# Performance work log

Measured on AMD Instinct MI355X. Metric: run time of the kernel, lower is better.

The kernel has to match this reference:

```python
import jax, jax.numpy as jnp
import numpy as np

ALPHA, BETA, GAMMA = 0.05, 0.95, 0.95   # list_weight
TANH_ALPHA = 2.0
GDEP = 2


def _gcn_rnn(x, adp, preA, W, b):
    # GCN type 'RNN': adaptive batched adj + predefined adj
    h = x
    outs = [h]
    for _ in range(GDEP):
        h = (ALPHA * x
             + BETA * jnp.einsum('nvc,nvw->nwc', h, adp)
             + GAMMA * jnp.einsum('nvc,vw->nwc', h, preA))
        outs.append(h)
    return jnp.concatenate(outs, -1) @ W + b


def _gcn_hyper(x, A, W, b):
    h = x
    outs = [h]
    for _ in range(GDEP):
        h = ALPHA * x + GAMMA * jnp.einsum('nvc,vw->nwc', h, A)
        outs.append(h)
    return jnp.concatenate(outs, -1) @ W + b


def _gcn_tgn(x, Ab, W, b):
    h = x
    outs = [h]
    for _ in range(GDEP):
        h = ALPHA * x + GAMMA * jnp.einsum('nvc,nvw->nwc', h, Ab)
        outs.append(h)
    return jnp.concatenate(outs, -1) @ W + b


def setup_inputs() -> dict:
    key = jax.random.key(0)
    ks = jax.random.split(key, 28)
    B, T, N, F = 16, 24, 512, 2
    H, E = 64, 16          # hidden_size, node embedding dim (dims_hyper[-1])
    TGN_OUT = 32
    D_ATTN = 4 * F         # TAttn default dim_out = 4 * dim_in
    p = lambda i, shape: jax.random.normal(ks[i], shape, dtype=jnp.float32) * 0.1
    return {
        'sample': jax.random.normal(ks[0], (B, T, N, F), dtype=jnp.float32),
        'predefined_A': jax.random.uniform(ks[1], (N, N), dtype=jnp.float32),
        'w_query': p(2, (F, D_ATTN)), 'w_key': p(3, (F, D_ATTN)),
        'attn_bias': p(4, (D_ATTN,)), 'attn_trans': p(5, (D_ATTN, 1)),
        'W_tgn': p(6, ((GDEP + 1) * F, TGN_OUT)), 'b_tgn': p(7, (TGN_OUT,)),
        'W_agg1': p(8, ((GDEP + 1) * H, E)), 'b_agg1': p(9, (E,)),
        'W_agg2': p(10, ((GDEP + 1) * H, E)), 'b_agg2': p(11, (E,)),
        'W_srcemb': p(12, (F, E)), 'b_srcemb': p(13, (E,)),
        'W_tgtemb': p(14, (F, E)), 'b_tgtemb': p(15, (E,)),
        'W_gz': p(16, ((GDEP + 1) * (F + H), H)), 'b_gz': p(17, (H,)),
        'W_gr': p(18, ((GDEP + 1) * (F + H), H)), 'b_gr': p(19, (H,)),
        'W_gc': p(20, ((GDEP + 1) * (F + H), H)), 'b_gc': p(21, (H,)),
        'W_short': p(22, (TGN_OUT, F)), 'b_short': p(23, (F,)),
        'W_long': p(24, (H, F)), 'b_long': p(25, (F,)),
        'W_mix': p(26, (TGN_OUT + H, F)), 'b_mix': p(27, (F,)),
    }


def reference(sample, predefined_A, w_query, w_key, attn_bias, attn_trans,
              W_tgn, b_tgn, W_agg1, b_agg1, W_agg2, b_agg2,
              W_srcemb, b_srcemb, W_tgtemb, b_tgtemb,
              W_gz, b_gz, W_gr, b_gr, W_gc, b_gc,
              W_short, b_short, W_long, b_long, W_mix, b_mix):
    B, T, N, F = sample.shape
    H = W_long.shape[0]
    A = predefined_A
    eye = jnp.eye(N, dtype=sample.dtype)

    def gru_step(hidden, graph):
        # hidden: [B,N,H], graph: [B,N,F]
        gs = _gcn_hyper(hidden, A, W_agg1, b_agg1)
        gt = _gcn_hyper(hidden, A, W_agg2, b_agg2)
        nv_s = jnp.tanh(TANH_ALPHA * (graph @ W_srcemb + b_srcemb) * gs)
        nv_t = jnp.tanh(TANH_ALPHA * (graph @ W_tgtemb + b_tgtemb) * gt)
        a = (jnp.einsum('bnd,bmd->bnm', nv_s, nv_t)
             - jnp.einsum('bnd,bmd->bnm', nv_t, nv_s))
        adp = jax.nn.relu(jnp.tanh(TANH_ALPHA * a)) + eye
        adp = adp / adp.sum(-1, keepdims=True)           # row-normalized [B,N,N]
        combined = jnp.concatenate([graph, hidden], -1)
        z = jax.nn.sigmoid(_gcn_rnn(combined, adp, A, W_gz, b_gz))
        r = jax.nn.sigmoid(_gcn_rnn(combined, adp, A, W_gr, b_gr))
        c = jnp.tanh(_gcn_rnn(jnp.concatenate([graph, r * hidden], -1), adp, A, W_gc, b_gc))
        return z * hidden + (1.0 - z) * c

    hidden = jnp.zeros((B, N, H), dtype=sample.dtype)
    graphs = jnp.moveaxis(sample[:, 0:T - 4:4], 1, 0)    # [T', B, N, F]
    hidden = jax.lax.scan(lambda h, g: (gru_step(h, g), None), hidden, graphs)[0]

    # temporal additive attention over the last 4 graphs (TAttn)
    src = sample[:, -4:]                                  # [B,4,N,F]
    tar = sample[:, -1]                                   # [B,N,F]
    q = (tar @ w_query)[:, None, :, None, :]              # [B,1,N,1,D]
    k = (src @ w_key)[:, :, None, :, :]                   # [B,4,1,N,D]
    scores = (jnp.tanh(q + k + attn_bias) @ attn_trans)[..., 0]   # [B,4,N,N]
    attn = jax.nn.softmax(scores, axis=-1)

    # single TGN layer: graph conv with (predefined + attention) adjacency
    Ab = A[None] + attn.reshape(-1, N, N)                 # [B*4,N,N]
    out = _gcn_tgn(src.reshape(-1, N, F), Ab, W_tgn, b_tgn)
    out = jax.nn.relu(out.reshape(B, 4, N, -1))
    tar = out.sum(axis=1)                                 # [B,N,TGN_OUT]

    gat_result = tar @ W_short + b_short                  # [B,N,F]
    hidden = gru_step(hidden, gat_result)
    gru_result = hidden @ W_long + b_long
    final_result = jnp.concatenate([tar, hidden], -1) @ W_mix + b_mix
    return gat_result, gru_result, final_result, attn
```

## Files before the change

kernel.cpp:

```cpp
#include <hip/hip_runtime.h>

#define ALPHA_C 0.05f
#define BETA_C  0.95f
#define GAMMA_C 0.95f

constexpr int B = 16, T = 24, N = 512, F = 2, H = 64, E = 16;
constexpr int DA = 8;
constexpr int CC = F + H;
constexpr int TGN_OC = 32;
constexpr int NPART = 4;

__device__ __forceinline__ float fast_rcp(float x) { return __builtin_amdgcn_rcpf(x); }
__device__ __forceinline__ float fast_tanh(float x) {
    return 1.0f - 2.0f * fast_rcp(__expf(2.0f * x) + 1.0f);
}
__device__ __forceinline__ float fast_sigmoid(float x) {
    return fast_rcp(1.0f + __expf(-x));
}

__global__ void scaleA_kernel(const float* __restrict__ A, float* __restrict__ K1)
{
    int i = blockIdx.x * 256 + threadIdx.x;
    K1[i] = GAMMA_C * A[i];
}

__global__ __launch_bounds__(256) void k2_kernel(const float* __restrict__ A,
                                                 float* __restrict__ K2)
{
    __shared__ float rows[16][258];
    __shared__ float cols[256][17];
    const int tid = threadIdx.x;
    const int r0 = blockIdx.y * 16, c0 = blockIdx.x * 16;
    const int rr = tid >> 4, cc = tid & 15;
    float acc = 0.f;
    for (int k0 = 0; k0 < N; k0 += 256) {
#pragma unroll
        for (int it = 0; it < 4; ++it) {
            int l = it * 256 + tid;
            int row = l >> 6, k4 = (l & 63) << 2;
            *(float4*)&rows[row][k4] = *(const float4*)(A + (size_t)(r0 + row) * N + k0 + k4);
        }
#pragma unroll
        for (int it = 0; it < 4; ++it) {
            int l = it * 256 + tid;
            int k = l >> 2, c4 = (l & 3) << 2;
            *(float4*)&cols[k][c4] = *(const float4*)(A + (size_t)(k0 + k) * N + c0 + c4);
        }
        __syncthreads();
#pragma unroll 8
        for (int k = 0; k < 256; ++k) acc += rows[rr][k] * cols[k][cc];
        __syncthreads();
    }
    size_t i = (size_t)(r0 + rr) * N + c0 + cc;
    K2[i] = GAMMA_C * ALPHA_C * A[i] + GAMMA_C * GAMMA_C * acc;
}

template<int GCOLS, bool INSUM, bool MPB>
__device__ __forceinline__ void bmm_core(
    float* __restrict__ out, const float* __restrict__ x, const float* __restrict__ in,
    const float* __restrict__ M, int b, int w0, int vq, int tid,
    float (*sh_m)[68], float (*sh_h)[68])
{
    constexpr int Crow = 64 + GCOLS;
    const size_t pstr = (size_t)B * N * Crow;
    const int cg = tid & 15;
    const int wg = tid >> 4;

    float acc[2][4] = {{0,0,0,0},{0,0,0,0}};
    float ag[2] = {0.f, 0.f};

    const float* Mb = M + (MPB ? (size_t)b * N * N : 0);
    const float* inb = in + (size_t)b * N * Crow;

    for (int vt = 0; vt < 2; ++vt) {
        const int v0 = vq * 128 + vt * 64;
#pragma unroll
        for (int it = 0; it < 2; ++it) {
            int l = it * 512 + tid;
            int row = l >> 4, c4 = (l & 15) << 2;
            *(float4*)&sh_m[row][c4] =
                *(const float4*)(Mb + (size_t)(v0 + row) * N + w0 + c4);
        }
        if (GCOLS == 2) {
            const float2* h0 = (const float2*)(inb + (size_t)v0 * Crow);
            for (int l = tid; l < 64 * 33; l += 512) {
                int row = l / 33, k = (l - row * 33) * 2;
                float2 v = h0[l];
                if (INSUM) {
#pragma unroll
                    for (int j = 1; j < NPART; ++j) {
                        float2 w = ((const float2*)(inb + (size_t)j * pstr + (size_t)v0 * Crow))[l];
                        v.x += w.x; v.y += w.y;
                    }
                }
                *(float2*)&sh_h[row][k] = v;
            }
        } else {
            const float4* h0 = (const float4*)(inb + (size_t)v0 * Crow);
#pragma unroll
            for (int it = 0; it < 2; ++it) {
                int l = it * 512 + tid;
                int row = l >> 4, k = (l & 15) << 2;
                float4 v = h0[l];
                if (INSUM) {
#pragma unroll
                    for (int j = 1; j < NPART; ++j) {
                        float4 w = ((const float4*)(inb + (size_t)j * pstr + (size_t)v0 * Crow))[l];
                        v.x += w.x; v.y += w.y; v.z += w.z; v.w += w.w;
                    }
                }
                *(float4*)&sh_h[row][k] = v;
            }
        }
        __syncthreads();
#pragma unroll 8
        for (int j = 0; j < 64; ++j) {
            float2 mv = *(const float2*)&sh_m[j][wg << 1];
            float4 hv = *(const float4*)&sh_h[j][cg << 2];
            acc[0][0] += mv.x * hv.x; acc[0][1] += mv.x * hv.y;
            acc[0][2] += mv.x * hv.z; acc[0][3] += mv.x * hv.w;
            acc[1][0] += mv.y * hv.x; acc[1][1] += mv.y * hv.y;
            acc[1][2] += mv.y * hv.z; acc[1][3] += mv.y * hv.w;
            if (GCOLS > 0 && cg < GCOLS) {
                float gv = sh_h[j][64 + cg];
                ag[0] += mv.x * gv; ag[1] += mv.y * gv;
            }
        }
        __syncthreads();
    }
    float* outp = out + (size_t)vq * pstr + (size_t)b * N * Crow;
    const float* xb = x + (size_t)b * N * Crow;
#pragma unroll
    for (int r = 0; r < 2; ++r) {
        const int w = w0 + (wg << 1) + r;
        const size_t base = (size_t)w * Crow + (cg << 2);
        if (GCOLS == 2) {
            float o0 = acc[r][0], o1 = acc[r][1], o2 = acc[r][2], o3 = acc[r][3];
            if (vq == 0) {
                o0 += ALPHA_C * xb[base];     o1 += ALPHA_C * xb[base + 1];
                o2 += ALPHA_C * xb[base + 2]; o3 += ALPHA_C * xb[base + 3];
            }
            float2 lo = {o0, o1}, hi = {o2, o3};
            *(float2*)(outp + base) = lo;
            *(float2*)(outp + base + 2) = hi;
            if (cg < GCOLS) {
                size_t gb = (size_t)w * Crow + 64 + cg;
                float v = ag[r];
                if (vq == 0) v += ALPHA_C * xb[gb];
                outp[gb] = v;
            }
        } else {
            float4 ov = {acc[r][0], acc[r][1], acc[r][2], acc[r][3]};
            if (vq == 0) {
                float4 xv = *(const float4*)(xb + base);
                ov.x += ALPHA_C * xv.x; ov.y += ALPHA_C * xv.y;
                ov.z += ALPHA_C * xv.z; ov.w += ALPHA_C * xv.w;
            }
            *(float4*)(outp + base) = ov;
        }
    }
}

template<bool INSUM>
__global__ __launch_bounds__(512) void bmm4_kernel(
    float* __restrict__ out, const float* __restrict__ x, const float* __restrict__ in,
    const float* __restrict__ M)
{
    __shared__ float sh_m[64][68];
    __shared__ float sh_h[64][68];
    bmm_core<2, INSUM, true>(out, x, in, M, blockIdx.z, blockIdx.x * 64, blockIdx.y,
                             threadIdx.x, sh_m, sh_h);
}

__global__ __launch_bounds__(512) void hyper_kernel(
    float* __restrict__ P1, float* __restrict__ P2, const float* __restrict__ hidden,
    const float* __restrict__ K1, const float* __restrict__ K2)
{
    __shared__ float sh_m[64][68];
    __shared__ float sh_h[64][68];
    int vq = blockIdx.y & 3, which = blockIdx.y >> 2;
    float* out = which ? P2 : P1;
    const float* M = which ? K2 : K1;
    bmm_core<0, false, false>(out, hidden, hidden, M, blockIdx.z, blockIdx.x * 64, vq,
                              threadIdx.x, sh_m, sh_h);
}

__global__ __launch_bounds__(256) void gsgt5_kernel(
    const float* __restrict__ hidden, const float* __restrict__ P1, const float* __restrict__ P2,
    const float* __restrict__ Wa1, const float* __restrict__ ba1,
    const float* __restrict__ Wa2, const float* __restrict__ ba2,
    const float* __restrict__ graph, long gstride,
    const float* __restrict__ Wsrc, const float* __restrict__ bsrc,
    const float* __restrict__ Wtgt, const float* __restrict__ btgt,
    float* __restrict__ nv_s, float* __restrict__ nv_t)
{
    constexpr size_t psH = (size_t)B * N * H;
    __shared__ float sh[16][196];
    __shared__ float W1t[16][196];
    __shared__ float W2t[16][196];
    const int tid = threadIdx.x;
    const int e = tid & 15;
    const int row = tid >> 4;
    const size_t nn0 = (size_t)blockIdx.x * 16;
    {
        int f4 = ((int)(nn0) + row) * 16 + e;
        float4 v = ((const float4*)hidden)[f4];
        *(float4*)&sh[row][e << 2] = v;
        float4 a = ((const float4*)P1)[f4];
#pragma unroll
        for (int j = 1; j < NPART; ++j) {
            float4 w = ((const float4*)(P1 + (size_t)j * psH))[f4];
            a.x += w.x; a.y += w.y; a.z += w.z; a.w += w.w;
        }
        *(float4*)&sh[row][64 + (e << 2)] = a;
        float4 c = ((const float4*)P2)[f4];
#pragma unroll
        for (int j = 1; j < NPART; ++j) {
            float4 w = ((const float4*)(P2 + (size_t)j * psH))[f4];
            c.x += w.x; c.y += w.y; c.z += w.z; c.w += w.w;
        }
        *(float4*)&sh[row][128 + (e << 2)] = c;
    }
    for (int l = tid; l < 768; l += 256) {
        int sk = l >> 2, q = l & 3;
        float4 w1 = ((const float4*)Wa1)[l];
        float4 w2 = ((const float4*)Wa2)[l];
        W1t[4 * q + 0][sk] = w1.x; W1t[4 * q + 1][sk] = w1.y;
        W1t[4 * q + 2][sk] = w1.z; W1t[4 * q + 3][sk] = w1.w;
        W2t[4 * q + 0][sk] = w2.x; W2t[4 * q + 1][sk] = w2.y;
        W2t[4 * q + 2][sk] = w2.z; W2t[4 * q + 3][sk] = w2.w;
    }
    __syncthreads();
    float gs = ba1[e], gt = ba2[e];
#pragma unroll 8
    for (int sk = 0; sk < 192; sk += 4) {
        float4 xv = *(const float4*)&sh[row][sk];
        float4 w1 = *(const float4*)&W1t[e][sk];
        float4 w2 = *(const float4*)&W2t[e][sk];
        gs += xv.x * w1.x + xv.y * w1.y + xv.z * w1.z + xv.w * w1.w;
        gt += xv.x * w2.x + xv.y * w2.y + xv.z * w2.z + xv.w * w2.w;
    }
    size_t nn = nn0 + row;
    int b = (int)(nn >> 9), n = (int)(nn & (N - 1));
    const float* g = graph + (size_t)b * gstride + (size_t)n * F;
    float g0 = g[0], g1 = g[1];
    float es = g0 * Wsrc[e] + g1 * Wsrc[E + e] + bsrc[e];
    float et = g0 * Wtgt[e] + g1 * Wtgt[E + e] + btgt[e];
    nv_s[nn * E + e] = fast_tanh(2.0f * es * gs);
    nv_t[nn * E + e] = fast_tanh(2.0f * et * gt);
}

__global__ __launch_bounds__(512) void adp3_kernel(
    const float* __restrict__ nv_s, const float* __restrict__ nv_t,
    const float* __restrict__ A,
    const float* __restrict__ hidden, const float* __restrict__ graph, long gstride,
    float* __restrict__ Mcomb, float* __restrict__ comb)
{
    __shared__ float red[8][4];
    __shared__ float tot[4];
    const int m = threadIdx.x;
    const int n0 = blockIdx.x * 4;
    const int b = blockIdx.y;
    const float4* sm = (const float4*)(nv_s + ((size_t)b * N + m) * E);
    const float4* tm = (const float4*)(nv_t + ((size_t)b * N + m) * E);
    const float4* sn = (const float4*)(nv_s + ((size_t)b * N + n0) * E);
    const float4* tn = (const float4*)(nv_t + ((size_t)b * N + n0) * E);
    float a1[4] = {0.f,0.f,0.f,0.f}, a2[4] = {0.f,0.f,0.f,0.f};
#pragma unroll
    for (int dd = 0; dd < 4; ++dd) {
        float4 smv = sm[dd], tmv = tm[dd];
#pragma unroll
        for (int r = 0; r < 4; ++r) {
            float4 snv = sn[r * 4 + dd], tnv = tn[r * 4 + dd];
            a1[r] += snv.x * tmv.x + snv.y * tmv.y + snv.z * tmv.z + snv.w * tmv.w;
            a2[r] += tnv.x * smv.x + tnv.y * smv.y + tnv.z * smv.z + tnv.w * smv.w;
        }
    }
    float p[4];
#pragma unroll
    for (int r = 0; r < 4; ++r) {
        float pv = fmaxf(fast_tanh(2.0f * (a1[r] - a2[r])), 0.0f);
        if (m == n0 + r) pv += 1.0f;
        p[r] = pv;
    }
    float sr[4] = {p[0], p[1], p[2], p[3]};
    for (int o = 32; o > 0; o >>= 1) {
#pragma unroll
        for (int r = 0; r < 4; ++r) sr[r] += __shfl_down(sr[r], o);
    }
    int wid = m >> 6, lane = m & 63;
    if (lane == 0) {
#pragma unroll
        for (int r = 0; r < 4; ++r) red[wid][r] = sr[r];
    }
    __syncthreads();
    if (m < 4) {
        float t = 0.f;
        for (int i = 0; i < 8; ++i) t += red[i][m];
        tot[m] = BETA_C * fast_rcp(t);
    }
    __syncthreads();
#pragma unroll
    for (int r = 0; r < 4; ++r)
        Mcomb[((size_t)b * N + n0 + r) * N + m] =
            GAMMA_C * A[(size_t)(n0 + r) * N + m] + p[r] * tot[r];
    if (m < 4 * CC) {
        int r = m / CC, k = m - r * CC;
        size_t nn = (size_t)b * N + n0 + r;
        float v;
        if (k < F) v = graph[(size_t)b * gstride + (size_t)(n0 + r) * F + k];
        else       v = hidden[nn * H + (k - F)];
        comb[nn * CC + k] = v;
    }
}

__device__ __forceinline__ void stage_xt(float (*Xt)[20], const float* __restrict__ base,
                                         const float* __restrict__ P1,
                                         const float* __restrict__ P2,
                                         size_t nn0, int tid)
{
    constexpr size_t psC = (size_t)B * N * CC;
    const float2* c2 = (const float2*)(base + nn0 * CC);
    const float2* p1b = (const float2*)(P1 + nn0 * CC);
    const float2* p2b = (const float2*)(P2 + nn0 * CC);
    for (int l = tid; l < 16 * 33; l += 256) {
        int row = l & 15, kp = l >> 4;
        int idx = row * 33 + kp;
        float2 v = c2[idx];
        Xt[2 * kp][row] = v.x; Xt[2 * kp + 1][row] = v.y;
        float2 a = p1b[idx];
#pragma unroll
        for (int j = 1; j < NPART; ++j) {
            float2 w = ((const float2*)(P1 + (size_t)j * psC + nn0 * CC))[idx];
            a.x += w.x; a.y += w.y;
        }
        Xt[66 + 2 * kp][row] = a.x; Xt[66 + 2 * kp + 1][row] = a.y;
        float2 c = p2b[idx];
#pragma unroll
        for (int j = 1; j < NPART; ++j) {
            float2 w = ((const float2*)(P2 + (size_t)j * psC + nn0 * CC))[idx];
            c.x += w.x; c.y += w.y;
        }
        Xt[132 + 2 * kp][row] = c.x; Xt[132 + 2 * kp + 1][row] = c.y;
    }
}

__global__ __launch_bounds__(256) void zr5_kernel(
    const float* __restrict__ comb, const float* __restrict__ P1, const float* __restrict__ P2,
    const float* __restrict__ Wgz, const float* __restrict__ bgz,
    const float* __restrict__ Wgr, const float* __restrict__ bgr,
    const float* __restrict__ hidden,
    float* __restrict__ z, float* __restrict__ comb2)
{
    __shared__ float Xt[198][20];
    __shared__ float Wl[66][128];
    const int tid = threadIdx.x;
    const size_t nn0 = (size_t)blockIdx.x * 16;

    stage_xt(Xt, comb, P1, P2, nn0, tid);

    const int cp = tid & 63;
    const int rg = tid >> 6;
    float2 bias = (cp < 32) ? *(const float2*)&bgz[2 * cp]
                            : *(const float2*)&bgr[2 * cp - 64];
    float acc[4][2];
#pragma unroll
    for (int r = 0; r < 4; ++r) { acc[r][0] = bias.x; acc[r][1] = bias.y; }

    for (int ch = 0; ch < 3; ++ch) {
        const int sk0 = ch * 66;
        for (int l = tid; l < 66 * 32; l += 256) {
            int j = l >> 5, q = l & 31;
            float4 w = (q < 16)
                ? ((const float4*)(Wgz + (size_t)(sk0 + j) * H))[q]
                : ((const float4*)(Wgr + (size_t)(sk0 + j) * H))[q - 16];
            *(float4*)&Wl[j][q << 2] = w;
        }
        __syncthreads();
#pragma unroll 6
        for (int j = 0; j < 66; ++j) {
            float4 xv = *(const float4*)&Xt[sk0 + j][rg << 2];
            float2 wv = *(const float2*)&Wl[j][cp << 1];
            acc[0][0] += xv.x * wv.x; acc[0][1] += xv.x * wv.y;
            acc[1][0] += xv.y * wv.x; acc[1][1] += xv.y * wv.y;
            acc[2][0] += xv.z * wv.x; acc[2][1] += xv.z * wv.y;
            acc[3][0] += xv.w * wv.x; acc[3][1] += xv.w * wv.y;
        }
        __syncthreads();
    }

    if (cp < 32) {
        const int oc = 2 * cp;
#pragma unroll
        for (int r = 0; r < 4; ++r) {
            size_t nn = nn0 + (rg << 2) + r;
            z[nn * H + oc]     = fast_sigmoid(acc[r][0]);
            z[nn * H + oc + 1] = fast_sigmoid(acc[r][1]);
        }
    } else {
        const int oc = 2 * cp - 64;
#pragma unroll
        for (int r = 0; r < 4; ++r) {
            size_t nn = nn0 + (rg << 2) + r;
            float h0 = hidden[nn * H + oc], h1 = hidden[nn * H + oc + 1];
            comb2[nn * CC + F + oc]     = fast_sigmoid(acc[r][0]) * h0;
            comb2[nn * CC + F + oc + 1] = fast_sigmoid(acc[r][1]) * h1;
        }
    }
    if (tid < 32) {
        int row = tid >> 1, f = tid & 1;
        comb2[(nn0 + row) * CC + f] = Xt[f][row];
    }
}

__global__ __launch_bounds__(256) void cup5_kernel(
    const float* __restrict__ comb2, const float* __restrict__ P1, const float* __restrict__ P2,
    const float* __restrict__ Wgc, const float* __restrict__ bgc,
    const float* __restrict__ z, float* __restrict__ hidden)
{
    __shared__ float Xt[198][20];
    __shared__ float Wl[66][64];
    const int tid = threadIdx.x;
    const size_t nn0 = (size_t)blockIdx.x * 16;

    stage_xt(Xt, comb2, P1, P2, nn0, tid);

    const int cp = tid & 31;
    const int rg = tid >> 5;
    float2 bias = *(const float2*)&bgc[2 * cp];
    float acc[2][2];
#pragma unroll
    for (int r = 0; r < 2; ++r) { acc[r][0] = bias.x; acc[r][1] = bias.y; }

    for (int ch = 0; ch < 3; ++ch) {
        const int sk0 = ch * 66;
        for (int l = tid; l < 66 * 16; l += 256) {
            int j = l >> 4, q = l & 15;
            float4 w = ((const float4*)(Wgc + (size_t)(sk0 + j) * H))[q];
            *(float4*)&Wl[j][q << 2] = w;
        }
        __syncthreads();
#pragma unroll 6
        for (int j = 0; j < 66; ++j) {
            float2 xv = *(const float2*)&Xt[sk0 + j][rg << 1];
            float2 wv = *(const float2*)&Wl[j][cp << 1];
            acc[0][0] += xv.x * wv.x; acc[0][1] += xv.x * wv.y;
            acc[1][0] += xv.y * wv.x; acc[1][1] += xv.y * wv.y;
        }
        __syncthreads();
    }

    const int oc = 2 * cp;
#pragma unroll
    for (int r = 0; r < 2; ++r) {
        size_t nn = nn0 + (rg << 1) + r;
        float cv0 = fast_tanh(acc[r][0]);
        float cv1 = fast_tanh(acc[r][1]);
        float zv0 = z[nn * H + oc],     ho0 = hidden[nn * H + oc];
        float zv1 = z[nn * H + oc + 1], ho1 = hidden[nn * H + oc + 1];
        hidden[nn * H + oc]     = zv0 * ho0 + (1.0f - zv0) * cv0;
        hidden[nn * H + oc + 1] = zv1 * ho1 + (1.0f - zv1) * cv1;
    }
}

__global__ void qk_kernel(const float* __restrict__ sample,
                          const float* __restrict__ wq, const float* __restrict__ wk,
                          const float* __restrict__ attn_bias,
                          float* __restrict__ q, float* __restrict__ kk)
{
    int idx = blockIdx.x * 256 + threadIdx.x;
    if (idx < B * N * DA) {
        int d = idx & 7;
        int n = (idx >> 3) & (N - 1);
        int b = idx >> 12;
        const float* tar = sample + (((size_t)b * T + (T - 1)) * N + n) * F;
        q[idx] = tar[0] * wq[d] + tar[1] * wq[DA + d] + attn_bias[d];
    } else {
        int j = idx - B * N * DA;
        int d = j & 7;
        int n = (j >> 3) & (N - 1);
        int t = (j >> 12) & 3;
        int b = j >> 14;
        const float* s = sample + (((size_t)b * T + (T - 4 + t)) * N + n) * F;
        kk[j] = s[0] * wk[d] + s[1] * wk[DA + d];
    }
}

__global__ __launch_bounds__(256) void scores3_kernel(
    const float* __restrict__ q, const float* __restrict__ kk,
    const float* __restrict__ trans, float* __restrict__ attn)
{
    int bt = blockIdx.y;
    int b = bt >> 2;
    int rbase = blockIdx.x * 16;
    int wid = threadIdx.x >> 6, lane = threadIdx.x & 63;
    const float* kkbt = kk + (size_t)bt * N * DA;
    float* attnbt = attn + (size_t)bt * N * N;
    float tr[8];
#pragma unroll
    for (int d = 0; d < 8; ++d) tr[d] = trans[d];
    for (int i = 0; i < 4; ++i) {
        int n = rbase + wid * 4 + i;
        const float* qp = q + ((size_t)b * N + n) * DA;
        float4 qa = *(const float4*)qp, qb = *(const float4*)(qp + 4);
        float ev[8]; float ssum = 0.f;
#pragma unroll
        for (int k = 0; k < 8; ++k) {
            const float* kp = kkbt + (size_t)(k * 64 + lane) * DA;
            float4 ka = *(const float4*)kp, kb = *(const float4*)(kp + 4);
            float s = fast_tanh(qa.x + ka.x) * tr[0] + fast_tanh(qa.y + ka.y) * tr[1]
                    + fast_tanh(qa.z + ka.z) * tr[2] + fast_tanh(qa.w + ka.w) * tr[3]
                    + fast_tanh(qb.x + kb.x) * tr[4] + fast_tanh(qb.y + kb.y) * tr[5]
                    + fast_tanh(qb.z + kb.z) * tr[6] + fast_tanh(qb.w + kb.w) * tr[7];
            ev[k] = __expf(s);
            ssum += ev[k];
        }
        for (int o = 32; o > 0; o >>= 1) ssum += __shfl_down(ssum, o);
        ssum = __shfl(ssum, 0);
        float rinv = fast_rcp(ssum);
#pragma unroll
        for (int k = 0; k < 8; ++k)
            attnbt[(size_t)n * N + k * 64 + lane] = ev[k] * rinv;
    }
}

__global__ __launch_bounds__(256) void tgn2_kernel(
    const float* __restrict__ A, const float* __restrict__ attn,
    const float* __restrict__ hbase, long hsB, long hsT,
    const float* __restrict__ xbase, long xsB, long xsT,
    float* __restrict__ out)
{
    __shared__ float sh_m[64][65];
    __shared__ float sh_h[64][2];
    int bt = blockIdx.y;
    int w0 = blockIdx.x * 64;
    int tid = threadIdx.x;
    int wl = tid >> 2, c = tid & 1, vh = (tid >> 1) & 1;
    const float* hp = hbase + (size_t)(bt >> 2) * hsB + (size_t)(bt & 3) * hsT;
    const float* ap = attn + (size_t)bt * N * N;
    float acc = 0.f;
    for (int vt = 0; vt < 8; ++vt) {
        int v0 = vt * 64;
#pragma unroll
        for (int it = 0; it < 16; ++it) {
            int l = it * 256 + tid;
            int vr = l >> 6, wc = l & 63;
            size_t gi = (size_t)(v0 + vr) * N + (w0 + wc);
            sh_m[wc][vr] = A[gi] + ap[gi];
        }
        if (tid < 128) sh_h[tid >> 1][tid & 1] = hp[(size_t)(v0 + (tid >> 1)) * F + (tid & 1)];
        __syncthreads();
#pragma unroll
        for (int jj = 0; jj < 32; ++jj) {
            int j = vh * 32 + jj;
            acc += sh_m[wl][j] * sh_h[j][c];
        }
        __syncthreads();
    }
    acc += __shfl_xor(acc, 2);
    if (vh == 0) {
        const float* xp = xbase + (size_t)(bt >> 2) * xsB + (size_t)(bt & 3) * xsT;
        out[((size_t)bt * N + w0 + wl) * F + c] =
            ALPHA_C * xp[(size_t)(w0 + wl) * F + c] + GAMMA_C * acc;
    }
}

__global__ __launch_bounds__(256) void tgn_out_gat_kernel(
    const float* __restrict__ sample,
    const float* __restrict__ th1, const float* __restrict__ th2,
    const float* __restrict__ Wt, const float* __restrict__ bt_,
    const float* __restrict__ Ws, const float* __restrict__ bs,
    float* __restrict__ tar32, float* __restrict__ out0)
{
    __shared__ float sh_t[8][33];
    const int tid = threadIdx.x;
    const int oc = tid & 31;
    const int r = tid >> 5;
    const size_t nn = (size_t)blockIdx.x * 8 + r;
    const int n = (int)(nn & (N - 1));
    const int b = (int)(nn >> 9);
    float acc = 0.f;
    for (int t = 0; t < 4; ++t) {
        int bt = b * 4 + t;
        const float* s = sample + (((size_t)b * T + (T - 4 + t)) * N + n) * F;
        size_t rr = ((size_t)bt * N + n) * F;
        float v = bt_[oc];
        v += s[0] * Wt[0 * TGN_OC + oc] + s[1] * Wt[1 * TGN_OC + oc];
        v += th1[rr] * Wt[2 * TGN_OC + oc] + th1[rr + 1] * Wt[3 * TGN_OC + oc];
        v += th2[rr] * Wt[4 * TGN_OC + oc] + th2[rr + 1] * Wt[5 * TGN_OC + oc];
        acc += fmaxf(v, 0.0f);
    }
    tar32[nn * TGN_OC + oc] = acc;
    sh_t[r][oc] = acc;
    __syncthreads();
    if (tid < 16) {
        int row = tid >> 1, f = tid & 1;
        size_t nn2 = (size_t)blockIdx.x * 8 + row;
        float g = bs[f];
#pragma unroll
        for (int k = 0; k < TGN_OC; ++k) g += sh_t[row][k] * Ws[(size_t)k * F + f];
        out0[nn2 * F + f] = g;
    }
}

__global__ void final_kernel(const float* __restrict__ hidden, const float* __restrict__ tar32,
                             const float* __restrict__ Wl, const float* __restrict__ bl,
                             const float* __restrict__ Wm, const float* __restrict__ bm,
                             float* __restrict__ dout_gru, float* __restrict__ dout_fin)
{
    int idx = blockIdx.x * 256 + threadIdx.x;
    int f = idx & 1;
    int nn = idx >> 1;
    const float* hp = hidden + (size_t)nn * H;
    const float* tp = tar32 + (size_t)nn * TGN_OC;
    float g = bl[f], fin = bm[f];
    for (int k = 0; k < H; ++k) g += hp[k] * Wl[(size_t)k * F + f];
    for (int k = 0; k < TGN_OC; ++k) fin += tp[k] * Wm[(size_t)k * F + f];
    for (int k = 0; k < H; ++k) fin += hp[k] * Wm[(size_t)(TGN_OC + k) * F + f];
    dout_gru[idx] = g;
    dout_fin[idx] = fin;
}

namespace {
struct Ptrs {
    const float *sample, *A, *wq, *wk, *attn_bias, *attn_trans, *Wt, *bt_;
    const float *Wa1, *ba1, *Wa2, *ba2, *Wsrc, *bsrc, *Wtgt, *btgt;
    const float *Wgz, *bgz, *Wgr, *bgr, *Wgc, *bgc, *Wsh, *bsh, *Wl, *bl, *Wm, *bm;
    float *hidden, *nvs, *nvt, *Mcomb, *K1, *K2, *comb, *comb2, *z, *P1, *P2;
    float *q, *kk, *th1, *th2, *tar32;
};

void gru_step(hipStream_t stream, const Ptrs& p, const float* graph, long gstride)
{
    dim3 bg(8, NPART, B);
    hyper_kernel<<<dim3(8, 2 * NPART, B), 512, 0, stream>>>(p.P1, p.P2, p.hidden, p.K1, p.K2);
    gsgt5_kernel<<<B * N / 16, 256, 0, stream>>>(
        p.hidden, p.P1, p.P2, p.Wa1, p.ba1, p.Wa2, p.ba2, graph, gstride,
        p.Wsrc, p.bsrc, p.Wtgt, p.btgt, p.nvs, p.nvt);
    adp3_kernel<<<dim3(N / 4, B), 512, 0, stream>>>(
        p.nvs, p.nvt, p.A, p.hidden, graph, gstride, p.Mcomb, p.comb);
    bmm4_kernel<false><<<bg, 512, 0, stream>>>(p.P1, p.comb, p.comb, p.Mcomb);
    bmm4_kernel<true><<<bg, 512, 0, stream>>>(p.P2, p.comb, p.P1, p.Mcomb);
    zr5_kernel<<<B * N / 16, 256, 0, stream>>>(
        p.comb, p.P1, p.P2, p.Wgz, p.bgz, p.Wgr, p.bgr, p.hidden, p.z, p.comb2);
    bmm4_kernel<false><<<bg, 512, 0, stream>>>(p.P1, p.comb2, p.comb2, p.Mcomb);
    bmm4_kernel<true><<<bg, 512, 0, stream>>>(p.P2, p.comb2, p.P1, p.Mcomb);
    cup5_kernel<<<B * N / 16, 256, 0, stream>>>(
        p.comb2, p.P1, p.P2, p.Wgc, p.bgc, p.z, p.hidden);
}
}

extern "C" void kernel_launch(void* const* d_in, const int* in_sizes, int n_in,
                              void* d_out, int out_size, void* d_ws, size_t ws_size,
                              hipStream_t stream)
{
    (void)in_sizes; (void)n_in; (void)out_size; (void)ws_size;
    Ptrs p;
    p.sample = (const float*)d_in[0];
    p.A      = (const float*)d_in[1];
    p.wq     = (const float*)d_in[2];
    p.wk     = (const float*)d_in[3];
    p.attn_bias  = (const float*)d_in[4];
    p.attn_trans = (const float*)d_in[5];
    p.Wt  = (const float*)d_in[6];
    p.bt_ = (const float*)d_in[7];
    p.Wa1 = (const float*)d_in[8];
    p.ba1 = (const float*)d_in[9];
    p.Wa2 = (const float*)d_in[10];
    p.ba2 = (const float*)d_in[11];
    p.Wsrc = (const float*)d_in[12];
    p.bsrc = (const float*)d_in[13];
    p.Wtgt = (const float*)d_in[14];
    p.btgt = (const float*)d_in[15];
    p.Wgz = (const float*)d_in[16];
    p.bgz = (const float*)d_in[17];
    p.Wgr = (const float*)d_in[18];
    p.bgr = (const float*)d_in[19];
    p.Wgc = (const float*)d_in[20];
    p.bgc = (const float*)d_in[21];
    p.Wsh = (const float*)d_in[22];
    p.bsh = (const float*)d_in[23];
    p.Wl  = (const float*)d_in[24];
    p.bl  = (const float*)d_in[25];
    p.Wm  = (const float*)d_in[26];
    p.bm  = (const float*)d_in[27];

    float* ws = (float*)d_ws;
    size_t off = 0;
    auto alloc = [&](size_t nelem) { float* r = ws + off; off += nelem; return r; };
    p.hidden = alloc((size_t)B * N * H);
    p.nvs    = alloc((size_t)B * N * E);
    p.nvt    = alloc((size_t)B * N * E);
    p.Mcomb  = alloc((size_t)B * N * N);
    p.K1     = alloc((size_t)N * N);
    p.K2     = alloc((size_t)N * N);
    p.comb   = alloc((size_t)B * N * CC);
    p.comb2  = alloc((size_t)B * N * CC);
    p.z      = alloc((size_t)B * N * H);
    p.P1     = alloc((size_t)NPART * B * N * CC);
    p.P2     = alloc((size_t)NPART * B * N * CC);
    p.q      = alloc((size_t)B * N * DA);
    p.kk     = alloc((size_t)B * 4 * N * DA);
    p.th1    = alloc((size_t)B * 4 * N * F);
    p.th2    = alloc((size_t)B * 4 * N * F);
    p.tar32  = alloc((size_t)B * N * TGN_OC);

    float* out = (float*)d_out;
    float* out_gat = out;
    float* out_gru = out + (size_t)B * N * F;
    float* out_fin = out + (size_t)2 * B * N * F;
    float* out_attn = out + (size_t)3 * B * N * F;

    hipMemsetAsync(p.hidden, 0, (size_t)B * N * H * sizeof(float), stream);
    scaleA_kernel<<<N * N / 256, 256, 0, stream>>>(p.A, p.K1);
    k2_kernel<<<dim3(32, 32), 256, 0, stream>>>(p.A, p.K2);

    for (int i = 0; i < 5; ++i) {
        const float* graph = p.sample + (size_t)(4 * i) * N * F;
        gru_step(stream, p, graph, (long)T * N * F);
    }

    qk_kernel<<<(B * N * DA + B * 4 * N * DA) / 256, 256, 0, stream>>>(
        p.sample, p.wq, p.wk, p.attn_bias, p.q, p.kk);
    scores3_kernel<<<dim3(32, 64), 256, 0, stream>>>(p.q, p.kk, p.attn_trans, out_attn);

    const float* srcbase = p.sample + (size_t)(T - 4) * N * F;
    tgn2_kernel<<<dim3(8, 64), 256, 0, stream>>>(
        p.A, out_attn, srcbase, (long)T * N * F, (long)N * F,
        srcbase, (long)T * N * F, (long)N * F, p.th1);
    tgn2_kernel<<<dim3(8, 64), 256, 0, stream>>>(
        p.A, out_attn, p.th1, (long)4 * N * F, (long)N * F,
        srcbase, (long)T * N * F, (long)N * F, p.th2);
    tgn_out_gat_kernel<<<B * N / 8, 256, 0, stream>>>(
        p.sample, p.th1, p.th2, p.Wt, p.bt_, p.Wsh, p.bsh, p.tar32, out_gat);

    gru_step(stream, p, out_gat, (long)N * F);

    final_kernel<<<(B * N * F) / 256, 256, 0, stream>>>(
        p.hidden, p.tar32, p.Wl, p.bl, p.Wm, p.bm, out_gru, out_fin);
}
```

Baseline: 1.270 ms.

## Enlarge per-thread register tiles in bmm kernels and fuse hyper K1/K2 passes

Measured after the change: 1.330 ms. 1.05x slower.

```diff
diff --git a/kernel.cpp b/kernel.cpp
--- a/kernel.cpp
+++ b/kernel.cpp
@@ -55,35 +55,38 @@
     K2[i] = GAMMA_C * ALPHA_C * A[i] + GAMMA_C * GAMMA_C * acc;
 }
 
-template<int GCOLS, bool INSUM, bool MPB>
-__device__ __forceinline__ void bmm_core(
+template<bool INSUM>
+__global__ __launch_bounds__(256) void bmm4_kernel(
     float* __restrict__ out, const float* __restrict__ x, const float* __restrict__ in,
-    const float* __restrict__ M, int b, int w0, int vq, int tid,
-    float (*sh_m)[68], float (*sh_h)[68])
-{
-    constexpr int Crow = 64 + GCOLS;
+    const float* __restrict__ M)
+{
+    __shared__ float sh_m[64][68];
+    __shared__ float sh_h[64][68];
+    constexpr int Crow = CC;
     const size_t pstr = (size_t)B * N * Crow;
+    const int tid = threadIdx.x;
+    const int b = blockIdx.z, w0 = blockIdx.x * 64, vq = blockIdx.y;
     const int cg = tid & 15;
     const int wg = tid >> 4;
 
-    float acc[2][4] = {{0,0,0,0},{0,0,0,0}};
-    float ag[2] = {0.f, 0.f};
-
-    const float* Mb = M + (MPB ? (size_t)b * N * N : 0);
+    float acc[4][4] = {{0,0,0,0},{0,0,0,0},{0,0,0,0},{0,0,0,0}};
+    float ag[4] = {0.f, 0.f, 0.f, 0.f};
+
+    const float* Mb = M + (size_t)b * N * N;
     const float* inb = in + (size_t)b * N * Crow;
 
     for (int vt = 0; vt < 2; ++vt) {
         const int v0 = vq * 128 + vt * 64;
 #pragma unroll
-        for (int it = 0; it < 2; ++it) {
-            int l = it * 512 + tid;
+        for (int it = 0; it < 4; ++it) {
+            int l = it * 256 + tid;
             int row = l >> 4, c4 = (l & 15) << 2;
             *(float4*)&sh_m[row][c4] =
                 *(const float4*)(Mb + (size_t)(v0 + row) * N + w0 + c4);
         }
-        if (GCOLS == 2) {
+        {
             const float2* h0 = (const float2*)(inb + (size_t)v0 * Crow);
-            for (int l = tid; l < 64 * 33; l += 512) {
+            for (int l = tid; l < 64 * 33; l += 256) {
                 int row = l / 33, k = (l - row * 33) * 2;
                 float2 v = h0[l];
                 if (INSUM) {
@@ -95,35 +98,24 @@
                 }
                 *(float2*)&sh_h[row][k] = v;
             }
-        } else {
-            const float4* h0 = (const float4*)(inb + (size_t)v0 * Crow);
-#pragma unroll
-            for (int it = 0; it < 2; ++it) {
-                int l = it * 512 + tid;
-                int row = l >> 4, k = (l & 15) << 2;
-                float4 v = h0[l];
-                if (INSUM) {
-#pragma unroll
-                    for (int j = 1; j < NPART; ++j) {
-                        float4 w = ((const float4*)(inb + (size_t)j * pstr + (size_t)v0 * Crow))[l];
-                        v.x += w.x; v.y += w.y; v.z += w.z; v.w += w.w;
-                    }
-                }
-                *(float4*)&sh_h[row][k] = v;
-            }
         }
         __syncthreads();
 #pragma unroll 8
         for (int j = 0; j < 64; ++j) {
-            float2 mv = *(const float2*)&sh_m[j][wg << 1];
+            float4 mv = *(const float4*)&sh_m[j][wg << 2];
             float4 hv = *(const float4*)&sh_h[j][cg << 2];
             acc[0][0] += mv.x * hv.x; acc[0][1] += mv.x * hv.y;
             acc[0][2] += mv.x * hv.z; acc[0][3] += mv.x * hv.w;
             acc[1][0] += mv.y * hv.x; acc[1][1] += mv.y * hv.y;
             acc[1][2] += mv.y * hv.z; acc[1][3] += mv.y * hv.w;
-            if (GCOLS > 0 && cg < GCOLS) {
+            acc[2][0] += mv.z * hv.x; acc[2][1] += mv.z * hv.y;
+            acc[2][2] += mv.z * hv.z; acc[2][3] += mv.z * hv.w;
+            acc[3][0] += mv.w * hv.x; acc[3][1] += mv.w * hv.y;
+            acc[3][2] += mv.w * hv.z; acc[3][3] += mv.w * hv.w;
+            if (cg < 2) {
                 float gv = sh_h[j][64 + cg];
                 ag[0] += mv.x * gv; ag[1] += mv.y * gv;
+                ag[2] += mv.z * gv; ag[3] += mv.w * gv;
             }
         }
         __syncthreads();
@@ -131,58 +123,99 @@
     float* outp = out + (size_t)vq * pstr + (size_t)b * N * Crow;
     const float* xb = x + (size_t)b * N * Crow;
 #pragma unroll
-    for (int r = 0; r < 2; ++r) {
-        const int w = w0 + (wg << 1) + r;
+    for (int r = 0; r < 4; ++r) {
+        const int w = w0 + (wg << 2) + r;
         const size_t base = (size_t)w * Crow + (cg << 2);
-        if (GCOLS == 2) {
-            float o0 = acc[r][0], o1 = acc[r][1], o2 = acc[r][2], o3 = acc[r][3];
-            if (vq == 0) {
-                o0 += ALPHA_C * xb[base];     o1 += ALPHA_C * xb[base + 1];
-                o2 += ALPHA_C * xb[base + 2]; o3 += ALPHA_C * xb[base + 3];
-            }
-            float2 lo = {o0, o1}, hi = {o2, o3};
-            *(float2*)(outp + base) = lo;
-            *(float2*)(outp + base + 2) = hi;
-            if (cg < GCOLS) {
-                size_t gb = (size_t)w * Crow + 64 + cg;
-                float v = ag[r];
-                if (vq == 0) v += ALPHA_C * xb[gb];
-                outp[gb] = v;
-            }
-        } else {
-            float4 ov = {acc[r][0], acc[r][1], acc[r][2], acc[r][3]};
-            if (vq == 0) {
-                float4 xv = *(const float4*)(xb + base);
-                ov.x += ALPHA_C * xv.x; ov.y += ALPHA_C * xv.y;
-                ov.z += ALPHA_C * xv.z; ov.w += ALPHA_C * xv.w;
-            }
-            *(float4*)(outp + base) = ov;
-        }
-    }
-}
-
-template<bool INSUM>
-__global__ __launch_bounds__(512) void bmm4_kernel(
-    float* __restrict__ out, const float* __restrict__ x, const float* __restrict__ in,
-    const float* __restrict__ M)
-{
-    __shared__ float sh_m[64][68];
-    __shared__ float sh_h[64][68];
-    bmm_core<2, INSUM, true>(out, x, in, M, blockIdx.z, blockIdx.x * 64, blockIdx.y,
-                             threadIdx.x, sh_m, sh_h);
-}
-
-__global__ __launch_bounds__(512) void hyper_kernel(
+        float o0 = acc[r][0], o1 = acc[r][1], o2 = acc[r][2], o3 = acc[r][3];
+        if (vq == 0) {
+            o0 += ALPHA_C * xb[base];     o1 += ALPHA_C * xb[base + 1];
+            o2 += ALPHA_C * xb[base + 2]; o3 += ALPHA_C * xb[base + 3];
+        }
+        float2 lo = {o0, o1}, hi = {o2, o3};
+        *(float2*)(outp + base) = lo;
+        *(float2*)(outp + base + 2) = hi;
+        if (cg < 2) {
+            size_t gb = (size_t)w * Crow + 64 + cg;
+            float v = ag[r];
+            if (vq == 0) v += ALPHA_C * xb[gb];
+            outp[gb] = v;
+        }
+    }
+}
+
+__global__ __launch_bounds__(256) void hyper2_kernel(
     float* __restrict__ P1, float* __restrict__ P2, const float* __restrict__ hidden,
     const float* __restrict__ K1, const float* __restrict__ K2)
 {
-    __shared__ float sh_m[64][68];
+    __shared__ float sh_m1[64][68];
+    __shared__ float sh_m2[64][68];
     __shared__ float sh_h[64][68];
-    int vq = blockIdx.y & 3, which = blockIdx.y >> 2;
-    float* out = which ? P2 : P1;
-    const float* M = which ? K2 : K1;
-    bmm_core<0, false, false>(out, hidden, hidden, M, blockIdx.z, blockIdx.x * 64, vq,
-                              threadIdx.x, sh_m, sh_h);
+    const size_t pstr = (size_t)B * N * H;
+    const int tid = threadIdx.x;
+    const int b = blockIdx.z, w0 = blockIdx.x * 64, vq = blockIdx.y;
+    const int cg = tid & 15;
+    const int wg = tid >> 4;
+
+    float a1[4][4] = {{0,0,0,0},{0,0,0,0},{0,0,0,0},{0,0,0,0}};
+    float a2[4][4] = {{0,0,0,0},{0,0,0,0},{0,0,0,0},{0,0,0,0}};
+    const float* inb = hidden + (size_t)b * N * H;
+
+    for (int vt = 0; vt < 2; ++vt) {
+        const int v0 = vq * 128 + vt * 64;
+#pragma unroll
+        for (int it = 0; it < 4; ++it) {
+            int l = it * 256 + tid;
+            int row = l >> 4, c4 = (l & 15) << 2;
+            *(float4*)&sh_m1[row][c4] =
+                *(const float4*)(K1 + (size_t)(v0 + row) * N + w0 + c4);
+            *(float4*)&sh_m2[row][c4] =
+                *(const float4*)(K2 + (size_t)(v0 + row) * N + w0 + c4);
+            *(float4*)&sh_h[row][c4] =
+                *(const float4*)(inb + (size_t)(v0 + row) * H + c4);
+        }
+        __syncthreads();
+#pragma unroll 4
+        for (int j = 0; j < 64; ++j) {
+            float4 hv = *(const float4*)&sh_h[j][cg << 2];
+            float4 m1 = *(const float4*)&sh_m1[j][wg << 2];
+            float4 m2 = *(const float4*)&sh_m2[j][wg << 2];
+            a1[0][0] += m1.x * hv.x; a1[0][1] += m1.x * hv.y;
+            a1[0][2] += m1.x * hv.z; a1[0][3] += m1.x * hv.w;
+            a1[1][0] += m1.y * hv.x; a1[1][1] += m1.y * hv.y;
+            a1[1][2] += m1.y * hv.z; a1[1][3] += m1.y * hv.w;
+            a1[2][0] += m1.z * hv.x; a1[2][1] += m1.z * hv.y;
+            a1[2][2] += m1.z * hv.z; a1[2][3] += m1.z * hv.w;
+            a1[3][0] += m1.w * hv.x; a1[3][1] += m1.w * hv.y;
+            a1[3][2] += m1.w * hv.z; a1[3][3] += m1.w * hv.w;
+            a2[0][0] += m2.x * hv.x; a2[0][1] += m2.x * hv.y;
+            a2[0][2] += m2.x * hv.z; a2[0][3] += m2.x * hv.w;
+            a2[1][0] += m2.y * hv.x; a2[1][1] += m2.y * hv.y;
+            a2[1][2] += m2.y * hv.z; a2[1][3] += m2.y * hv.w;
+            a2[2][0] += m2.z * hv.x; a2[2][1] += m2.z * hv.y;
+            a2[2][2] += m2.z * hv.z; a2[2][3] += m2.z * hv.w;
+            a2[3][0] += m2.w * hv.x; a2[3][1] += m2.w * hv.y;
+            a2[3][2] += m2.w * hv.z; a2[3][3] += m2.w * hv.w;
+        }
+        __syncthreads();
+    }
+    float* o1 = P1 + (size_t)vq * pstr + (size_t)b * N * H;
+    float* o2 = P2 + (size_t)vq * pstr + (size_t)b * N * H;
+#pragma unroll
+    for (int r = 0; r < 4; ++r) {
+        const int w = w0 + (wg << 2) + r;
+        const size_t base = (size_t)w * H + (cg << 2);
+        float4 v1 = {a1[r][0], a1[r][1], a1[r][2], a1[r][3]};
+        float4 v2 = {a2[r][0], a2[r][1], a2[r][2], a2[r][3]};
+        if (vq == 0) {
+            float4 xv = *(const float4*)(inb + base);
+            v1.x += ALPHA_C * xv.x; v1.y += ALPHA_C * xv.y;
+            v1.z += ALPHA_C * xv.z; v1.w += ALPHA_C * xv.w;
+            v2.x += ALPHA_C * xv.x; v2.y += ALPHA_C * xv.y;
+            v2.z += ALPHA_C * xv.z; v2.w += ALPHA_C * xv.w;
+        }
+        *(float4*)(o1 + base) = v1;
+        *(float4*)(o2 + base) = v2;
+    }
 }
 
 __global__ __launch_bounds__(256) void gsgt5_kernel(
@@ -633,18 +666,18 @@
 void gru_step(hipStream_t stream, const Ptrs& p, const float* graph, long gstride)
 {
     dim3 bg(8, NPART, B);
-    hyper_kernel<<<dim3(8, 2 * NPART, B), 512, 0, stream>>>(p.P1, p.P2, p.hidden, p.K1, p.K2);
+    hyper2_kernel<<<bg, 256, 0, stream>>>(p.P1, p.P2, p.hidden, p.K1, p.K2);
     gsgt5_kernel<<<B * N / 16, 256, 0, stream>>>(
         p.hidden, p.P1, p.P2, p.Wa1, p.ba1, p.Wa2, p.ba2, graph, gstride,
         p.Wsrc, p.bsrc, p.Wtgt, p.btgt, p.nvs, p.nvt);
     adp3_kernel<<<dim3(N / 4, B), 512, 0, stream>>>(
         p.nvs, p.nvt, p.A, p.hidden, graph, gstride, p.Mcomb, p.comb);
-    bmm4_kernel<false><<<bg, 512, 0, stream>>>(p.P1, p.comb, p.comb, p.Mcomb);
-    bmm4_kernel<true><<<bg, 512, 0, stream>>>(p.P2, p.comb, p.P1, p.Mcomb);
+    bmm4_kernel<false><<<bg, 256, 0, stream>>>(p.P1, p.comb, p.comb, p.Mcomb);
+    bmm4_kernel<true><<<bg, 256, 0, stream>>>(p.P2, p.comb, p.P1, p.Mcomb);
     zr5_kernel<<<B * N / 16, 256, 0, stream>>>(
         p.comb, p.P1, p.P2, p.Wgz, p.bgz, p.Wgr, p.bgr, p.hidden, p.z, p.comb2);
-    bmm4_kernel<false><<<bg, 512, 0, stream>>>(p.P1, p.comb2, p.comb2, p.Mcomb);
-    bmm4_kernel<true><<<bg, 512, 0, stream>>>(p.P2, p.comb2, p.P1, p.Mcomb);
+    bmm4_kernel<false><<<bg, 256, 0, stream>>>(p.P1, p.comb2, p.comb2, p.Mcomb);
+    bmm4_kernel<true><<<bg, 256, 0, stream>>>(p.P2, p.comb2, p.P1, p.Mcomb);
     cup5_kernel<<<B * N / 16, 256, 0, stream>>>(
         p.comb2, p.P1, p.P2, p.Wgc, p.bgc, p.z, p.hidden);
 }
```
